# Optimization experiments

Measured on AMD Instinct MI355X. Metric: run time of the kernel, lower is better.

Reference implementation:

```python
import jax, jax.numpy as jnp
import numpy as np

# OFDM/MIMO constants from the source module
N = 512        # subcarriers
N_R = 2        # rx antennas
N_T = 2        # tx antennas
M_BITS = 4     # bits per QAM symbol (16-QAM)
CP = 7         # cyclic prefix = IsiDuration - 1
NO = 1e-5
EBNO_DB = 10.0
BATCH = 4096

# unit-average-power 16-QAM: per-axis levels, index = re_idx + 4*im_idx, bits LSB-first
LEV = jnp.asarray(np.array([-3.0, -1.0, 1.0, 3.0], np.float32) / np.sqrt(10.0))
_idx = np.arange(2 ** M_BITS)
CONST = jnp.asarray(((np.array([-3., -1., 1., 3.]) / np.sqrt(10.))[_idx % 4]
                     + 1j * (np.array([-3., -1., 1., 3.]) / np.sqrt(10.))[_idx // 4]).astype(np.complex64))


def setup_inputs() -> dict:
    key = jax.random.key(0)
    k1, k2, k3 = jax.random.split(key, 3)
    y_data_nld = jax.random.normal(k1, (BATCH, N_R, N + CP, 2), jnp.float32)
    y_ls = jax.random.normal(k2, (BATCH, N_R, N + CP, 2), jnp.float32)
    x_ls_idx = jax.random.randint(k3, (BATCH, N_T, N), 0, 2 ** M_BITS)
    return {"y_data_nld": y_data_nld, "y_ls": y_ls, "x_ls_idx": x_ls_idx}


def _c(x):
    return jax.lax.complex(x[..., 0], x[..., 1])


def _interp_c(xq, xp, fp):
    # fp: [M, P] complex -> [M, N] complex, linear interp per row (np.interp semantics)
    return jax.vmap(lambda fr, fi: jnp.interp(xq, xp, fr) + 1j * jnp.interp(xq, xp, fi))(fp.real, fp.imag)


def _forward(y_data_nld, y_ls, x_ls_idx):
    B = y_data_nld.shape[0]
    pi = 10.0 ** (EBNO_DB / 10.0) * NO * N          # = 0.0512
    sqrt_pi = jnp.sqrt(jnp.float32(pi))

    # strip CP, FFT, normalize (1/N * fft)
    Y = jnp.fft.fft(_c(y_data_nld)[..., CP:], axis=-1) / N            # [B, N_r, N]
    Y_l = jnp.fft.fft(_c(y_ls)[..., CP:], axis=-1) / (N * sqrt_pi)     # [B, N_r, N]

    x_ls = CONST[x_ls_idx]                                             # [B, N_t, N] pilots

    # comb-type LS estimates + linear interpolation to all N subcarriers
    xq = jnp.arange(N, dtype=jnp.float32)
    H_t = []
    for t in range(N_T):
        comb = jnp.arange(t, N, N_T)                                   # pilot subcarriers for tx t
        pil = Y_l[:, :, comb] / x_ls[:, None, t, comb]                 # [B, N_r, N/N_t]
        if t == 0:
            xp = jnp.concatenate([comb, jnp.array([N - 1])]).astype(jnp.float32)
            fp = jnp.concatenate([pil, pil[..., -1:]], axis=-1)
        else:
            xp = jnp.concatenate([jnp.array([0]), comb]).astype(jnp.float32)
            fp = jnp.concatenate([pil[..., :1], pil], axis=-1)
        P = fp.shape[-1]
        H_t.append(_interp_c(xq, xp, fp.reshape(B * N_R, P)).reshape(B, N_R, N))
    Hm = jnp.stack(H_t, axis=-1)                                       # [B, N_r, N, N_t]
    Hm = jnp.transpose(Hm, (0, 2, 1, 3))                               # [B, N, N_r, N_t]

    # per-subcarrier 2x2 linear solve: X_hat = H^{-1} Y / sqrt(pi)
    X_hat = jnp.linalg.solve(Hm, jnp.transpose(Y, (0, 2, 1))[..., None])[..., 0] / sqrt_pi  # [B, N, N_t]
    x_hat_ri = jnp.stack([X_hat.real, X_hat.imag], axis=-1)            # [B, N, N_t, 2]

    # nearest-QAM demap (square 16-QAM: per-axis argmin == joint argmin), bits LSB-first
    vre = jnp.argmin((X_hat.real[..., None] - LEV) ** 2, axis=-1)      # [B, N, N_t]
    vim = jnp.argmin((X_hat.imag[..., None] - LEV) ** 2, axis=-1)
    qidx = vre + 4 * vim
    bits = (qidx[..., None] >> jnp.arange(M_BITS)) & 1                 # [B, N, N_t, m]
    b_hat = jnp.transpose(bits, (0, 2, 1, 3)).reshape(B, N_T, N * M_BITS).astype(jnp.float32)
    return x_hat_ri, b_hat


def reference(y_data_nld, y_ls, x_ls_idx):
    return _forward(y_data_nld, y_ls, x_ls_idx)
```

## Files before the change

### kernel.cpp

```cpp
#include <hip/hip_runtime.h>

namespace {

constexpr int NSC  = 512;
constexpr int CP   = 7;
constexpr int NTOT = 519;

__device__ __forceinline__ int p2(int x) { return x + (x >> 4); }
__device__ __forceinline__ int p4(int x) { return x + (x >> 4); }

typedef float f4 __attribute__((ext_vector_type(4)));

struct cf { float x, y; };
__device__ __forceinline__ cf cadd(cf a, cf b) { return {a.x + b.x, a.y + b.y}; }
__device__ __forceinline__ cf csub(cf a, cf b) { return {a.x - b.x, a.y - b.y}; }
__device__ __forceinline__ cf cmul(cf a, cf b) { return {a.x*b.x - a.y*b.y, a.x*b.y + a.y*b.x}; }
__device__ __forceinline__ cf mni(cf a) { return {a.y, -a.x}; }

__device__ __forceinline__ void fft8(cf a[8]) {
    const float s = 0.70710678118654752f;
    cf b0 = a[0], b1 = a[4], b2 = a[2], b3 = a[6];
    cf b4 = a[1], b5 = a[5], b6 = a[3], b7 = a[7];
    cf c0 = cadd(b0, b1), c1 = csub(b0, b1);
    cf c2 = cadd(b2, b3), c3 = csub(b2, b3);
    cf c4 = cadd(b4, b5), c5 = csub(b4, b5);
    cf c6 = cadd(b6, b7), c7 = csub(b6, b7);
    cf d0 = cadd(c0, c2), d2 = csub(c0, c2);
    cf d1 = cadd(c1, mni(c3)), d3 = csub(c1, mni(c3));
    cf d4 = cadd(c4, c6), d6 = csub(c4, c6);
    cf d5 = cadd(c5, mni(c7)), d7 = csub(c5, mni(c7));
    cf e5 = { s * (d5.x + d5.y), s * (d5.y - d5.x) };
    cf e6 = mni(d6);
    cf e7 = { s * (d7.y - d7.x), -s * (d7.x + d7.y) };
    a[0] = cadd(d0, d4); a[4] = csub(d0, d4);
    a[1] = cadd(d1, e5); a[5] = csub(d1, e5);
    a[2] = cadd(d2, e6); a[6] = csub(d2, e6);
    a[3] = cadd(d3, e7); a[7] = csub(d3, e7);
}

__global__ __launch_bounds__(256, 8) void ofdm_mimo_kernel(
    const float* __restrict__ y_data,
    const float* __restrict__ y_ls,
    const int*   __restrict__ x_idx,
    float*       __restrict__ out,
    int B)
{
    __shared__ cf sb[4][544];

    const int b   = blockIdx.x;
    const int tid = threadIdx.x;
    const int q   = tid >> 6;
    const int t   = tid & 63;

    const float sc = (float)(1.0 / (512.0 * 0.22627416997969522));

    const float W64A  = -6.2831853071795864769f / 64.0f;
    const float W512A = -6.2831853071795864769f / 512.0f;

    const float lev[4] = {-0.9486832980505138f, -0.31622776601683794f,
                           0.31622776601683794f, 0.9486832980505138f};
    float pxr[2], pxi[2], pinv[2];
    #pragma unroll
    for (int j = 0; j < 2; ++j) {
        int comb = j + 2 * tid;
        int idx = x_idx[((size_t)(b * 2 + j)) * NSC + comb];
        float xr = lev[idx & 3];
        float xi = lev[(idx >> 2) & 3];
        pxr[j] = xr; pxi[j] = xi;
        pinv[j] = 1.0f / (xr * xr + xi * xi);
    }

    const int r = q & 1;
    const float* srcp = (q < 2) ? y_data : y_ls;
    const float2* xin = (const float2*)(srcp + ((size_t)(b * 2 + r) * NTOT + CP) * 2);

    cf a[8];
    #pragma unroll
    for (int n2 = 0; n2 < 8; ++n2) {
        float2 v = xin[t + 64 * n2];
        a[n2] = { v.x * sc, v.y * sc };
    }
    fft8(a);

    {
        const int n1 = t >> 3;
        float sn, cs;
        __sincosf(W64A * (float)n1, &sn, &cs);
        cf w1 = {cs, sn}, w = w1;
        #pragma unroll
        for (int k0 = 1; k0 < 8; ++k0) {
            a[k0] = cmul(a[k0], w);
            w = cmul(w, w1);
        }
    }
    #pragma unroll
    for (int k0 = 0; k0 < 8; ++k0) sb[q][p2(t * 8 + k0)] = a[k0];
    __builtin_amdgcn_wave_barrier();

    #pragma unroll
    for (int n1 = 0; n1 < 8; ++n1)
        a[n1] = sb[q][p2(n1 * 64 + (t & 7) * 8 + (t >> 3))];
    __builtin_amdgcn_wave_barrier();
    fft8(a);

    {
        const int n0 = t & 7, k0 = t >> 3;
        float sn, cs, sn2, cs2;
        __sincosf(W512A * (float)(n0 * k0), &sn, &cs);
        __sincosf(W64A * (float)n0, &sn2, &cs2);
        cf w = {cs, sn}, st = {cs2, sn2};
        #pragma unroll
        for (int k1 = 0; k1 < 8; ++k1) {
            a[k1] = cmul(a[k1], w);
            w = cmul(w, st);
        }
    }
    #pragma unroll
    for (int k1 = 0; k1 < 8; ++k1)
        sb[q][p2((t & 7) * 64 + (t >> 3) * 8 + k1)] = a[k1];
    __builtin_amdgcn_wave_barrier();

    #pragma unroll
    for (int n0 = 0; n0 < 8; ++n0)
        a[n0] = sb[q][p2(n0 * 64 + (t >> 3) * 8 + (t & 7))];
    __builtin_amdgcn_wave_barrier();
    fft8(a);

    #pragma unroll
    for (int k2 = 0; k2 < 8; ++k2)
        sb[q][p2((t >> 3) + 8 * (t & 7) + 64 * k2)] = a[k2];
    __syncthreads();

    float4 pout[2];
    #pragma unroll
    for (int j = 0; j < 2; ++j) {
        int comb = j + 2 * tid;
        int pc = p2(comb);
        cf y0l = sb[2][pc];
        cf y1l = sb[3][pc];
        pout[j] = make_float4((y0l.x * pxr[j] + y0l.y * pxi[j]) * pinv[j],
                              (y0l.y * pxr[j] - y0l.x * pxi[j]) * pinv[j],
                              (y1l.x * pxr[j] + y1l.y * pxi[j]) * pinv[j],
                              (y1l.y * pxr[j] - y1l.x * pxi[j]) * pinv[j]);
    }
    __syncthreads();
    {
        float4* pilA = (float4*)sb[2];
        float4* pilB = (float4*)sb[3];
        pilA[p4(tid)] = pout[0];
        pilB[p4(tid)] = pout[1];
    }
    __syncthreads();

    const float4* pilA = (const float4*)sb[2];
    const float4* pilB = (const float4*)sb[3];
    #pragma unroll
    for (int ni = 0; ni < 2; ++ni) {
        const int n = tid + 256 * ni;
        const int kp = n >> 1;
        const int kR = (kp + 1 < 256) ? kp + 1 : 255;
        const int kL = (kp - 1 > 0) ? kp - 1 : 0;
        const float wA = (n & 1) ? 0.5f : 0.0f;
        const float wB = (n & 1) ? 0.0f : 0.5f;

        float4 L0 = pilA[p4(kp)];
        float4 R0 = pilA[p4(kR)];
        float4 R1 = pilB[p4(kp)];
        float4 L1 = pilB[p4(kL)];

        cf H00 = { L0.x + wA * (R0.x - L0.x), L0.y + wA * (R0.y - L0.y) };
        cf H10 = { L0.z + wA * (R0.z - L0.z), L0.w + wA * (R0.w - L0.w) };
        cf H01 = { R1.x + wB * (L1.x - R1.x), R1.y + wB * (L1.y - R1.y) };
        cf H11 = { R1.z + wB * (L1.z - R1.z), R1.w + wB * (L1.w - R1.w) };

        cf Y0 = sb[0][p2(n)];
        cf Y1 = sb[1][p2(n)];

        cf det  = csub(cmul(H00, H11), cmul(H01, H10));
        cf num0 = csub(cmul(H11, Y0), cmul(H01, Y1));
        cf num1 = csub(cmul(H00, Y1), cmul(H10, Y0));
        float invden = 1.0f / (det.x * det.x + det.y * det.y);
        float X0r = (num0.x * det.x + num0.y * det.y) * invden;
        float X0i = (num0.y * det.x - num0.x * det.y) * invden;
        float X1r = (num1.x * det.x + num1.y * det.y) * invden;
        float X1i = (num1.y * det.x - num1.x * det.y) * invden;

        f4 xv = { X0r, X0i, X1r, X1i };
        __builtin_nontemporal_store(xv, (f4*)(out + (size_t)b * 2048 + (size_t)n * 4));

        const float bnd = 0.63245553203367587f;
        auto qi = [&](float v) -> int {
            return (v <= -bnd) ? 0 : (v <= 0.0f) ? 1 : (v <= bnd) ? 2 : 3;
        };
        int vre0 = qi(X0r), vim0 = qi(X0i);
        int vre1 = qi(X1r), vim1 = qi(X1i);

        size_t bbase = (size_t)B * 2048;
        f4 b0v = { (float)(vre0 & 1), (float)((vre0 >> 1) & 1),
                   (float)(vim0 & 1), (float)((vim0 >> 1) & 1) };
        __builtin_nontemporal_store(
            b0v, (f4*)(out + bbase + ((size_t)b * 2 + 0) * 2048 + (size_t)n * 4));
        f4 b1v = { (float)(vre1 & 1), (float)((vre1 >> 1) & 1),
                   (float)(vim1 & 1), (float)((vim1 >> 1) & 1) };
        __builtin_nontemporal_store(
            b1v, (f4*)(out + bbase + ((size_t)b * 2 + 1) * 2048 + (size_t)n * 4));
    }
}

}

extern "C" void kernel_launch(void* const* d_in, const int* in_sizes, int n_in,
                              void* d_out, int out_size, void* d_ws, size_t ws_size,
                              hipStream_t stream) {
    const float* y_data = (const float*)d_in[0];
    const float* y_ls   = (const float*)d_in[1];
    const int*   x_idx  = (const int*)d_in[2];
    float* out = (float*)d_out;

    int B = in_sizes[0] / (2 * NTOT * 2);
    ofdm_mimo_kernel<<<B, 256, 0, stream>>>(y_data, y_ls, x_idx, out, B);
}
```

Before: 35.32 us.

## Process two batches per block with software-prefetched inputs for the next batch

Each block now handles two batch items with a grid-stride loop, loading the next item's time samples and pilot indices into registers while the current FFT and solve run. The aim is to hide global load latency behind compute and cut the block count in half. Nontemporal stores become plain float4 stores, and the launch-bounds occupancy hint drops from 8 to 6 to make room for the extra registers. The grid is B/NB, so B must be divisible by 2, and the lower occupancy may cost latency hiding elsewhere.

```diff
diff --git a/kernel.cpp b/kernel.cpp
--- a/kernel.cpp
+++ b/kernel.cpp
@@ -5,11 +5,10 @@
 constexpr int NSC  = 512;
 constexpr int CP   = 7;
 constexpr int NTOT = 519;
+constexpr int NB   = 2;
 
 __device__ __forceinline__ int p2(int x) { return x + (x >> 4); }
 __device__ __forceinline__ int p4(int x) { return x + (x >> 4); }
-
-typedef float f4 __attribute__((ext_vector_type(4)));
 
 struct cf { float x, y; };
 __device__ __forceinline__ cf cadd(cf a, cf b) { return {a.x + b.x, a.y + b.y}; }
@@ -38,7 +37,7 @@
     a[3] = cadd(d3, e7); a[7] = csub(d3, e7);
 }
 
-__global__ __launch_bounds__(256, 8) void ofdm_mimo_kernel(
+__global__ __launch_bounds__(256, 6) void ofdm_mimo_kernel(
     const float* __restrict__ y_data,
     const float* __restrict__ y_ls,
     const int*   __restrict__ x_idx,
@@ -47,10 +46,11 @@
 {
     __shared__ cf sb[4][544];
 
-    const int b   = blockIdx.x;
     const int tid = threadIdx.x;
     const int q   = tid >> 6;
     const int t   = tid & 63;
+    const int r   = q & 1;
+    const int stride = gridDim.x;
 
     const float sc = (float)(1.0 / (512.0 * 0.22627416997969522));
 
@@ -59,151 +59,175 @@
 
     const float lev[4] = {-0.9486832980505138f, -0.31622776601683794f,
                            0.31622776601683794f, 0.9486832980505138f};
-    float pxr[2], pxi[2], pinv[2];
+
+    const float* srcp = (q < 2) ? y_data : y_ls;
+
+    float2 xv[8];
+    int idxc[2];
+    {
+        const int b = blockIdx.x;
+        const float2* xin = (const float2*)(srcp + ((size_t)(b * 2 + r) * NTOT + CP) * 2);
+        #pragma unroll
+        for (int n2 = 0; n2 < 8; ++n2) xv[n2] = xin[t + 64 * n2];
+        #pragma unroll
+        for (int j = 0; j < 2; ++j)
+            idxc[j] = x_idx[((size_t)(b * 2 + j)) * NSC + j + 2 * tid];
+    }
+
     #pragma unroll
-    for (int j = 0; j < 2; ++j) {
-        int comb = j + 2 * tid;
-        int idx = x_idx[((size_t)(b * 2 + j)) * NSC + comb];
-        float xr = lev[idx & 3];
-        float xi = lev[(idx >> 2) & 3];
-        pxr[j] = xr; pxi[j] = xi;
-        pinv[j] = 1.0f / (xr * xr + xi * xi);
-    }
-
-    const int r = q & 1;
-    const float* srcp = (q < 2) ? y_data : y_ls;
-    const float2* xin = (const float2*)(srcp + ((size_t)(b * 2 + r) * NTOT + CP) * 2);
-
-    cf a[8];
-    #pragma unroll
-    for (int n2 = 0; n2 < 8; ++n2) {
-        float2 v = xin[t + 64 * n2];
-        a[n2] = { v.x * sc, v.y * sc };
-    }
-    fft8(a);
-
-    {
-        const int n1 = t >> 3;
-        float sn, cs;
-        __sincosf(W64A * (float)n1, &sn, &cs);
-        cf w1 = {cs, sn}, w = w1;
-        #pragma unroll
-        for (int k0 = 1; k0 < 8; ++k0) {
-            a[k0] = cmul(a[k0], w);
-            w = cmul(w, w1);
-        }
-    }
-    #pragma unroll
-    for (int k0 = 0; k0 < 8; ++k0) sb[q][p2(t * 8 + k0)] = a[k0];
-    __builtin_amdgcn_wave_barrier();
-
-    #pragma unroll
-    for (int n1 = 0; n1 < 8; ++n1)
-        a[n1] = sb[q][p2(n1 * 64 + (t & 7) * 8 + (t >> 3))];
-    __builtin_amdgcn_wave_barrier();
-    fft8(a);
-
-    {
-        const int n0 = t & 7, k0 = t >> 3;
-        float sn, cs, sn2, cs2;
-        __sincosf(W512A * (float)(n0 * k0), &sn, &cs);
-        __sincosf(W64A * (float)n0, &sn2, &cs2);
-        cf w = {cs, sn}, st = {cs2, sn2};
-        #pragma unroll
-        for (int k1 = 0; k1 < 8; ++k1) {
-            a[k1] = cmul(a[k1], w);
-            w = cmul(w, st);
-        }
-    }
-    #pragma unroll
-    for (int k1 = 0; k1 < 8; ++k1)
-        sb[q][p2((t & 7) * 64 + (t >> 3) * 8 + k1)] = a[k1];
-    __builtin_amdgcn_wave_barrier();
-
-    #pragma unroll
-    for (int n0 = 0; n0 < 8; ++n0)
-        a[n0] = sb[q][p2(n0 * 64 + (t >> 3) * 8 + (t & 7))];
-    __builtin_amdgcn_wave_barrier();
-    fft8(a);
-
-    #pragma unroll
-    for (int k2 = 0; k2 < 8; ++k2)
-        sb[q][p2((t >> 3) + 8 * (t & 7) + 64 * k2)] = a[k2];
-    __syncthreads();
-
-    float4 pout[2];
-    #pragma unroll
-    for (int j = 0; j < 2; ++j) {
-        int comb = j + 2 * tid;
-        int pc = p2(comb);
-        cf y0l = sb[2][pc];
-        cf y1l = sb[3][pc];
-        pout[j] = make_float4((y0l.x * pxr[j] + y0l.y * pxi[j]) * pinv[j],
-                              (y0l.y * pxr[j] - y0l.x * pxi[j]) * pinv[j],
-                              (y1l.x * pxr[j] + y1l.y * pxi[j]) * pinv[j],
-                              (y1l.y * pxr[j] - y1l.x * pxi[j]) * pinv[j]);
-    }
-    __syncthreads();
-    {
-        float4* pilA = (float4*)sb[2];
-        float4* pilB = (float4*)sb[3];
-        pilA[p4(tid)] = pout[0];
-        pilB[p4(tid)] = pout[1];
-    }
-    __syncthreads();
-
-    const float4* pilA = (const float4*)sb[2];
-    const float4* pilB = (const float4*)sb[3];
-    #pragma unroll
-    for (int ni = 0; ni < 2; ++ni) {
-        const int n = tid + 256 * ni;
-        const int kp = n >> 1;
-        const int kR = (kp + 1 < 256) ? kp + 1 : 255;
-        const int kL = (kp - 1 > 0) ? kp - 1 : 0;
-        const float wA = (n & 1) ? 0.5f : 0.0f;
-        const float wB = (n & 1) ? 0.0f : 0.5f;
-
-        float4 L0 = pilA[p4(kp)];
-        float4 R0 = pilA[p4(kR)];
-        float4 R1 = pilB[p4(kp)];
-        float4 L1 = pilB[p4(kL)];
-
-        cf H00 = { L0.x + wA * (R0.x - L0.x), L0.y + wA * (R0.y - L0.y) };
-        cf H10 = { L0.z + wA * (R0.z - L0.z), L0.w + wA * (R0.w - L0.w) };
-        cf H01 = { R1.x + wB * (L1.x - R1.x), R1.y + wB * (L1.y - R1.y) };
-        cf H11 = { R1.z + wB * (L1.z - R1.z), R1.w + wB * (L1.w - R1.w) };
-
-        cf Y0 = sb[0][p2(n)];
-        cf Y1 = sb[1][p2(n)];
-
-        cf det  = csub(cmul(H00, H11), cmul(H01, H10));
-        cf num0 = csub(cmul(H11, Y0), cmul(H01, Y1));
-        cf num1 = csub(cmul(H00, Y1), cmul(H10, Y0));
-        float invden = 1.0f / (det.x * det.x + det.y * det.y);
-        float X0r = (num0.x * det.x + num0.y * det.y) * invden;
-        float X0i = (num0.y * det.x - num0.x * det.y) * invden;
-        float X1r = (num1.x * det.x + num1.y * det.y) * invden;
-        float X1i = (num1.y * det.x - num1.x * det.y) * invden;
-
-        f4 xv = { X0r, X0i, X1r, X1i };
-        __builtin_nontemporal_store(xv, (f4*)(out + (size_t)b * 2048 + (size_t)n * 4));
-
-        const float bnd = 0.63245553203367587f;
-        auto qi = [&](float v) -> int {
-            return (v <= -bnd) ? 0 : (v <= 0.0f) ? 1 : (v <= bnd) ? 2 : 3;
-        };
-        int vre0 = qi(X0r), vim0 = qi(X0i);
-        int vre1 = qi(X1r), vim1 = qi(X1i);
-
-        size_t bbase = (size_t)B * 2048;
-        f4 b0v = { (float)(vre0 & 1), (float)((vre0 >> 1) & 1),
-                   (float)(vim0 & 1), (float)((vim0 >> 1) & 1) };
-        __builtin_nontemporal_store(
-            b0v, (f4*)(out + bbase + ((size_t)b * 2 + 0) * 2048 + (size_t)n * 4));
-        f4 b1v = { (float)(vre1 & 1), (float)((vre1 >> 1) & 1),
-                   (float)(vim1 & 1), (float)((vim1 >> 1) & 1) };
-        __builtin_nontemporal_store(
-            b1v, (f4*)(out + bbase + ((size_t)b * 2 + 1) * 2048 + (size_t)n * 4));
+    for (int ib = 0; ib < NB; ++ib) {
+        const int b = blockIdx.x + ib * stride;
+
+        cf a[8];
+        #pragma unroll
+        for (int n2 = 0; n2 < 8; ++n2) a[n2] = { xv[n2].x * sc, xv[n2].y * sc };
+        fft8(a);
+
+        {
+            const int n1 = t >> 3;
+            float sn, cs;
+            __sincosf(W64A * (float)n1, &sn, &cs);
+            cf w1 = {cs, sn}, w = w1;
+            #pragma unroll
+            for (int k0 = 1; k0 < 8; ++k0) {
+                a[k0] = cmul(a[k0], w);
+                w = cmul(w, w1);
+            }
+        }
+        #pragma unroll
+        for (int k0 = 0; k0 < 8; ++k0) sb[q][p2(t * 8 + k0)] = a[k0];
+
+        float2 xv2[8];
+        int idxn[2];
+        if (ib + 1 < NB) {
+            const int bn = b + stride;
+            const float2* xin = (const float2*)(srcp + ((size_t)(bn * 2 + r) * NTOT + CP) * 2);
+            #pragma unroll
+            for (int n2 = 0; n2 < 8; ++n2) xv2[n2] = xin[t + 64 * n2];
+            #pragma unroll
+            for (int j = 0; j < 2; ++j)
+                idxn[j] = x_idx[((size_t)(bn * 2 + j)) * NSC + j + 2 * tid];
+        }
+        __builtin_amdgcn_wave_barrier();
+
+        #pragma unroll
+        for (int n1 = 0; n1 < 8; ++n1)
+            a[n1] = sb[q][p2(n1 * 64 + (t & 7) * 8 + (t >> 3))];
+        __builtin_amdgcn_wave_barrier();
+        fft8(a);
+
+        {
+            const int n0 = t & 7, k0 = t >> 3;
+            float sn, cs, sn2, cs2;
+            __sincosf(W512A * (float)(n0 * k0), &sn, &cs);
+            __sincosf(W64A * (float)n0, &sn2, &cs2);
+            cf w = {cs, sn}, st = {cs2, sn2};
+            #pragma unroll
+            for (int k1 = 0; k1 < 8; ++k1) {
+                a[k1] = cmul(a[k1], w);
+                w = cmul(w, st);
+            }
+        }
+        #pragma unroll
+        for (int k1 = 0; k1 < 8; ++k1)
+            sb[q][p2((t & 7) * 64 + (t >> 3) * 8 + k1)] = a[k1];
+        __builtin_amdgcn_wave_barrier();
+
+        #pragma unroll
+        for (int n0 = 0; n0 < 8; ++n0)
+            a[n0] = sb[q][p2(n0 * 64 + (t >> 3) * 8 + (t & 7))];
+        __builtin_amdgcn_wave_barrier();
+        fft8(a);
+
+        #pragma unroll
+        for (int k2 = 0; k2 < 8; ++k2)
+            sb[q][p2((t >> 3) + 8 * (t & 7) + 64 * k2)] = a[k2];
+        __syncthreads();
+
+        float4 pout[2];
+        #pragma unroll
+        for (int j = 0; j < 2; ++j) {
+            int comb = j + 2 * tid;
+            int pc = p2(comb);
+            int idx = idxc[j];
+            float xr = lev[idx & 3];
+            float xi = lev[(idx >> 2) & 3];
+            float inv = 1.0f / (xr * xr + xi * xi);
+            cf y0l = sb[2][pc];
+            cf y1l = sb[3][pc];
+            pout[j] = make_float4((y0l.x * xr + y0l.y * xi) * inv,
+                                  (y0l.y * xr - y0l.x * xi) * inv,
+                                  (y1l.x * xr + y1l.y * xi) * inv,
+                                  (y1l.y * xr - y1l.x * xi) * inv);
+        }
+        __syncthreads();
+        {
+            float4* pilA = (float4*)sb[2];
+            float4* pilB = (float4*)sb[3];
+            pilA[p4(tid)] = pout[0];
+            pilB[p4(tid)] = pout[1];
+        }
+        __syncthreads();
+
+        const float4* pilA = (const float4*)sb[2];
+        const float4* pilB = (const float4*)sb[3];
+        #pragma unroll
+        for (int ni = 0; ni < 2; ++ni) {
+            const int n = tid + 256 * ni;
+            const int kp = n >> 1;
+            const int kR = (kp + 1 < 256) ? kp + 1 : 255;
+            const int kL = (kp - 1 > 0) ? kp - 1 : 0;
+            const float wA = (n & 1) ? 0.5f : 0.0f;
+            const float wB = (n & 1) ? 0.0f : 0.5f;
+
+            float4 L0 = pilA[p4(kp)];
+            float4 R0 = pilA[p4(kR)];
+            float4 R1 = pilB[p4(kp)];
+            float4 L1 = pilB[p4(kL)];
+
+            cf H00 = { L0.x + wA * (R0.x - L0.x), L0.y + wA * (R0.y - L0.y) };
+            cf H10 = { L0.z + wA * (R0.z - L0.z), L0.w + wA * (R0.w - L0.w) };
+            cf H01 = { R1.x + wB * (L1.x - R1.x), R1.y + wB * (L1.y - R1.y) };
+            cf H11 = { R1.z + wB * (L1.z - R1.z), R1.w + wB * (L1.w - R1.w) };
+
+            cf Y0 = sb[0][p2(n)];
+            cf Y1 = sb[1][p2(n)];
+
+            cf det  = csub(cmul(H00, H11), cmul(H01, H10));
+            cf num0 = csub(cmul(H11, Y0), cmul(H01, Y1));
+            cf num1 = csub(cmul(H00, Y1), cmul(H10, Y0));
+            float invden = 1.0f / (det.x * det.x + det.y * det.y);
+            float X0r = (num0.x * det.x + num0.y * det.y) * invden;
+            float X0i = (num0.y * det.x - num0.x * det.y) * invden;
+            float X1r = (num1.x * det.x + num1.y * det.y) * invden;
+            float X1i = (num1.y * det.x - num1.x * det.y) * invden;
+
+            *(float4*)(out + (size_t)b * 2048 + (size_t)n * 4) =
+                make_float4(X0r, X0i, X1r, X1i);
+
+            const float bnd = 0.63245553203367587f;
+            auto qi = [&](float v) -> int {
+                return (v <= -bnd) ? 0 : (v <= 0.0f) ? 1 : (v <= bnd) ? 2 : 3;
+            };
+            int vre0 = qi(X0r), vim0 = qi(X0i);
+            int vre1 = qi(X1r), vim1 = qi(X1i);
+
+            size_t bbase = (size_t)B * 2048;
+            *(float4*)(out + bbase + ((size_t)b * 2 + 0) * 2048 + (size_t)n * 4) =
+                make_float4((float)(vre0 & 1), (float)((vre0 >> 1) & 1),
+                            (float)(vim0 & 1), (float)((vim0 >> 1) & 1));
+            *(float4*)(out + bbase + ((size_t)b * 2 + 1) * 2048 + (size_t)n * 4) =
+                make_float4((float)(vre1 & 1), (float)((vre1 >> 1) & 1),
+                            (float)(vim1 & 1), (float)((vim1 >> 1) & 1));
+        }
+
+        if (ib + 1 < NB) {
+            __syncthreads();
+            #pragma unroll
+            for (int n2 = 0; n2 < 8; ++n2) xv[n2] = xv2[n2];
+            idxc[0] = idxn[0];
+            idxc[1] = idxn[1];
+        }
     }
 }
 
@@ -218,5 +242,5 @@
     float* out = (float*)d_out;
 
     int B = in_sizes[0] / (2 * NTOT * 2);
-    ofdm_mimo_kernel<<<B, 256, 0, stream>>>(y_data, y_ls, x_idx, out, B);
-}
+    ofdm_mimo_kernel<<<B / NB, 256, 0, stream>>>(y_data, y_ls, x_idx, out, B);
+}
```

Result: slower. 102.0 us (+188.8%).
